# Kernel tuning notes

Measured on AMD Instinct MI355X. Metric: run time of the kernel, lower is better.

## Reference

```python
import jax, jax.numpy as jnp
import numpy as np

DIM = 512
NUM_HEADS = 8
HEAD_DIM = DIM // NUM_HEADS
SCALE = HEAD_DIM ** -0.5
B, T = 8, 1024


def setup_inputs() -> dict:
    key = jax.random.key(0)
    ks = jax.random.split(key, 6)
    x = jax.random.normal(ks[0], (B, T, DIM), dtype=jnp.float32)
    attn_mask = jax.random.randint(ks[1], (B, T, T), 0, 2) == 1  # bool [B,T,T]
    s = 1.0 / np.sqrt(DIM)
    qkv_w = jax.random.uniform(ks[2], (3 * DIM, DIM), jnp.float32, -s, s)
    qkv_b = jax.random.uniform(ks[3], (3 * DIM,), jnp.float32, -s, s)
    proj_w = jax.random.uniform(ks[4], (DIM, DIM), jnp.float32, -s, s)
    proj_b = jax.random.uniform(ks[5], (DIM,), jnp.float32, -s, s)
    return {"x": x, "attn_mask": attn_mask, "qkv_w": qkv_w, "qkv_b": qkv_b,
            "proj_w": proj_w, "proj_b": proj_b}


def reference(x, attn_mask, qkv_w, qkv_b, proj_w, proj_b):
    b, t, c = x.shape
    # QKV projection (torch Linear: x @ W.T + b), split into q,k,v heads
    qkv = x @ qkv_w.T + qkv_b                      # [b,t,3*c]
    qkv = qkv.reshape(b, t, 3, NUM_HEADS, HEAD_DIM)
    qkv = jnp.transpose(qkv, (2, 0, 3, 1, 4))      # [3,b,h,t,d]
    q, k, v = qkv[0], qkv[1], qkv[2]
    scores = jnp.einsum('bhqd,bhkd->bhqk', q, k) * SCALE  # [b,h,t,t]
    min_val = jnp.finfo(scores.dtype).min
    scores = jnp.where(attn_mask[:, None, :, :], min_val, scores)
    attn = jax.nn.softmax(scores, axis=-1)
    out = jnp.einsum('bhqk,bhkd->bhqd', attn, v)   # [b,h,t,d]
    out = jnp.transpose(out, (0, 2, 1, 3)).reshape(b, t, c)
    return out @ proj_w.T + proj_b
```

## Files before the change

kernel.cpp:

```cpp
#include <hip/hip_runtime.h>
#include <math.h>

#define DIM   512
#define NH    8
#define HD    64
#define BATCH 8
#define SEQ   1024
#define QSCALE 0.18033688011112042f

typedef unsigned short u16;
typedef unsigned int   u32;
typedef unsigned long long u64;
typedef __bf16 bf16x8 __attribute__((ext_vector_type(8)));
typedef float  f32x4  __attribute__((ext_vector_type(4)));

__device__ inline u16 f2bf(float f) {
  u32 u = __builtin_bit_cast(u32, f);
  return (u16)((u + 0x7fffu + ((u >> 16) & 1u)) >> 16);
}
__device__ inline float bf2f(u16 h) {
  return __builtin_bit_cast(float, (u32)h << 16);
}
__device__ inline u32 pk2(float a, float b) {
  return (u32)f2bf(a) | ((u32)f2bf(b) << 16);
}

__device__ inline void a16(const u16* g, u16* l) {
  __builtin_amdgcn_global_load_lds(
      (const __attribute__((address_space(1))) u32*)g,
      (__attribute__((address_space(3))) u32*)l, 16, 0, 0);
}


__device__ inline void decomp_body(const float* __restrict__ src, u16* ph,
                                   u16* pl, int t) {
  #pragma unroll
  for (int c = 0; c < 4; ++c) {
    const int cid = c * 256 + t;
    const int row = cid & 15, kc = cid >> 4;
    float f[8];
    *(float4*)&f[0] = *(const float4*)&src[row * DIM + kc * 8];
    *(float4*)&f[4] = *(const float4*)&src[row * DIM + kc * 8 + 4];
    u16 hv[8], lv[8];
    #pragma unroll
    for (int j = 0; j < 8; ++j) {
      hv[j] = f2bf(f[j]);
      lv[j] = f2bf(f[j] - bf2f(hv[j]));
    }
    *(uint4*)&ph[(size_t)cid * 8] = *(const uint4*)hv;
    *(uint4*)&pl[(size_t)cid * 8] = *(const uint4*)lv;
  }
}

__global__ __launch_bounds__(256) void prep(
    const int* __restrict__ mask, u64* __restrict__ bits,
    const float* __restrict__ x, u16* __restrict__ xhi, u16* __restrict__ xlo,
    const float* __restrict__ qkvw, u16* __restrict__ wqh, u16* __restrict__ wql,
    const float* __restrict__ projw, u16* __restrict__ wph, u16* __restrict__ wpl) {
  const int blk = blockIdx.x;
  const int t = threadIdx.x;
  if (blk < 32768) {
    const size_t gid = (size_t)blk * 256 + t;
    const int lane = t & 63;
    const size_t w = gid >> 6;
    const int v = mask[w * 64 + lane];
    const u64 b = __ballot(v != 0);
    if (lane == 0) {
      const int bb = (int)(w >> 14), q = (int)((w >> 4) & 1023),
                kt = (int)(w & 15);
      bits[(((size_t)(bb << 4 | kt)) << 10) | q] = b;
    }
  } else if (blk < 33280) {
    const int rg = blk - 32768;
    decomp_body(x + (size_t)rg * 16 * DIM, xhi + (size_t)rg * 8192,
                xlo + (size_t)rg * 8192, t);
  } else if (blk < 33376) {
    const int rg = blk - 33280;
    decomp_body(qkvw + (size_t)rg * 16 * DIM, wqh + (size_t)rg * 8192,
                wql + (size_t)rg * 8192, t);
  } else {
    const int rg = blk - 33376;
    decomp_body(projw + (size_t)rg * 16 * DIM, wph + (size_t)rg * 8192,
                wpl + (size_t)rg * 8192, t);
  }
}

template <int MB, bool QKV>
__global__ __launch_bounds__(256, 3) void mfma_gemm(
    const u16* __restrict__ Agh, const u16* __restrict__ Agl,
    const u16* __restrict__ Bgh, const u16* __restrict__ Bgl,
    const float* __restrict__ bias, void* __restrict__ out0,
    u16* __restrict__ kfr, u16* __restrict__ vfr) {
  __shared__ u16 sAh[2][MB * 1024];
  __shared__ u16 sAl[2][MB * 1024];

  const int tid = threadIdx.x;
  const int lane = tid & 63;
  const int wv = tid >> 6;
  const int lk = lane & 15, lq = lane >> 4;
  const int m0 = blockIdx.x * (32 * MB), n0 = blockIdx.y * 128;
  const int wm = (wv & 1) * MB;
  const int wn = (wv >> 1) * 4;

  const u16* gAh = Agh + (size_t)(m0 >> 4) * 8192 + lane * 8;
  const u16* gAl = Agl + (size_t)(m0 >> 4) * 8192 + lane * 8;
  const u16* gB0h = Bgh + ((size_t)((n0 >> 4) + wn)) * 8192 + lane * 8;
  const u16* gB0l = Bgl + ((size_t)((n0 >> 4) + wn)) * 8192 + lane * 8;

  auto stageA = [&](int bufi, int ki) {
    #pragma unroll
    for (int it = 0; it < MB / 2; ++it) {
      const int t = it * 4 + wv;
      const size_t go = (size_t)t * 8192 + (size_t)ki * 512;
      const int lo_ = t * 512 + lane * 8;
      a16(gAh + go, &sAh[bufi][lo_]);
      a16(gAl + go, &sAl[bufi][lo_]);
    }
  };

  f32x4 acc[MB][4];
  #pragma unroll
  for (int i = 0; i < MB; ++i)
    #pragma unroll
    for (int j = 0; j < 4; ++j) acc[i][j] = (f32x4){0.f, 0.f, 0.f, 0.f};

  stageA(0, 0);
  __syncthreads();

  #pragma unroll 1
  for (int ki = 0; ki < 16; ++ki) {
    const int cur = ki & 1;
    bf16x8 bh[4], bl[4];
    #pragma unroll
    for (int j = 0; j < 4; ++j) {
      bh[j] = *(const bf16x8*)(gB0h + (size_t)j * 8192 + (size_t)ki * 512);
      bl[j] = *(const bf16x8*)(gB0l + (size_t)j * 8192 + (size_t)ki * 512);
    }
    bf16x8 ah[MB], al[MB];
    #pragma unroll
    for (int i = 0; i < MB; ++i) {
      ah[i] = *(const bf16x8*)&sAh[cur][(wm + i) * 512 + lane * 8];
      al[i] = *(const bf16x8*)&sAl[cur][(wm + i) * 512 + lane * 8];
    }
    if (ki < 15) stageA(cur ^ 1, ki + 1);
    __builtin_amdgcn_sched_barrier(0);

    __builtin_amdgcn_s_setprio(1);
    #pragma unroll
    for (int i = 0; i < MB; ++i)
      #pragma unroll
      for (int j = 0; j < 4; ++j) {
        acc[i][j] = __builtin_amdgcn_mfma_f32_16x16x32_bf16(ah[i], bh[j], acc[i][j], 0, 0, 0);
        acc[i][j] = __builtin_amdgcn_mfma_f32_16x16x32_bf16(ah[i], bl[j], acc[i][j], 0, 0, 0);
        acc[i][j] = __builtin_amdgcn_mfma_f32_16x16x32_bf16(al[i], bh[j], acc[i][j], 0, 0, 0);
      }
    __builtin_amdgcn_s_setprio(0);

    __syncthreads();
  }

  #pragma unroll
  for (int j = 0; j < 4; ++j) {
    const int n = n0 + (wn + j) * 16 + lk;
    const float bv_ = bias[n];
    #pragma unroll
    for (int i = 0; i < MB; ++i) {
      const int mb = m0 + (wm + i) * 16 + lq * 4;
      if (QKV) {
        const int which = n >> 9, h = (n >> 6) & 7, d = n & 63;
        const int b = mb >> 10, tok0 = mb & 1023;
        const size_t hb = (size_t)((b << 3) + h) << 16;
        if (which == 2) {
          const size_t base = hb + ((size_t)(tok0 >> 6) << 12) +
                              ((size_t)((d >> 4) & 3) << 10) +
                              ((size_t)((tok0 >> 5) & 1) << 9) +
                              ((size_t)((d & 15) + (((tok0 >> 3) & 3) << 4)) << 3) +
                              (size_t)(tok0 & 7);
          uint2 o2;
          o2.x = pk2(acc[i][j][0] + bv_, acc[i][j][1] + bv_);
          o2.y = pk2(acc[i][j][2] + bv_, acc[i][j][3] + bv_);
          *(uint2*)&vfr[base] = o2;
        } else if (which == 1) {
          const size_t base = hb + ((size_t)(tok0 >> 4) << 10) +
                              ((size_t)(d >> 5) << 9) + (size_t)(d & 7) +
                              ((size_t)(((d >> 3) & 3) << 4) << 3);
          #pragma unroll
          for (int r = 0; r < 4; ++r)
            kfr[base + (((tok0 & 15) + r) << 3)] = f2bf(acc[i][j][r] + bv_);
        } else {
          u16* dst = (u16*)out0;
          #pragma unroll
          for (int r = 0; r < 4; ++r)
            dst[(((size_t)((b << 3) + h) << 10 | (tok0 + r)) << 6) + d] =
                f2bf((acc[i][j][r] + bv_) * QSCALE);
        }
      } else {
        #pragma unroll
        for (int r = 0; r < 4; ++r)
          ((float*)out0)[(size_t)(mb + r) * DIM + n] = acc[i][j][r] + bv_;
      }
    }
  }
}

__global__ __launch_bounds__(256) void attn_mfma(
    const u16* __restrict__ qg, const u16* __restrict__ kfr,
    const u16* __restrict__ vfr, const u64* __restrict__ bitsT,
    u16* __restrict__ ohi, u16* __restrict__ olo) {
  __shared__ u16 Kls[2][4096];
  __shared__ u16 Vls[2][4096];
  __shared__ u16 Ps[64 * 72];

  const int tid = threadIdx.x;
  const int lane = tid & 63;
  const int wv = tid >> 6;
  const int lk = lane & 15, lq = lane >> 4;
  const int bh = blockIdx.x;
  const int q0 = blockIdx.y * 64;
  const int bb = bh >> 3;
  const int q = q0 + wv * 16 + lk;

  const u16* qrow = qg + ((size_t)(bh << 10 | q) << 6);
  const bf16x8 bq0 = *(const bf16x8*)(qrow + lq * 8);
  const bf16x8 bq1 = *(const bf16x8*)(qrow + 32 + lq * 8);

  const u16* kh = kfr + ((size_t)bh << 16);
  const u16* vh = vfr + ((size_t)bh << 16);
  const u64* bitp = bitsT + ((size_t)bb << 14) + q;
  u16* pw = &Ps[(wv * 16 + lk) * 72];

  auto stage = [&](int bufi, int kt) {
    #pragma unroll
    for (int it = 0; it < 2; ++it) {
      const int c = it * 4 + wv;
      const int off = c * 512 + lane * 8;
      a16(kh + ((size_t)kt << 12) + off, &Kls[bufi][off]);
      a16(vh + ((size_t)kt << 12) + off, &Vls[bufi][off]);
    }
  };

  f32x4 o_[4];
  float l = 0.f;
  #pragma unroll
  for (int t = 0; t < 4; ++t) o_[t] = (f32x4){0.f, 0.f, 0.f, 0.f};

  stage(0, 0);
  __syncthreads();

  #pragma unroll 1
  for (int kt = 0; kt < 16; ++kt) {
    const int cur = kt & 1;
    const u64 wd = bitp[(size_t)kt << 10];

    bf16x8 ak0[4], ak1[4], vb0[4], vb1[4];
    #pragma unroll
    for (int t = 0; t < 4; ++t) {
      ak0[t] = *(const bf16x8*)&Kls[cur][t * 1024 + lane * 8];
      ak1[t] = *(const bf16x8*)&Kls[cur][t * 1024 + 512 + lane * 8];
      vb0[t] = *(const bf16x8*)&Vls[cur][t * 1024 + lane * 8];
      vb1[t] = *(const bf16x8*)&Vls[cur][t * 1024 + 512 + lane * 8];
    }
    if (kt < 15) stage(cur ^ 1, kt + 1);
    __builtin_amdgcn_sched_barrier(0);

    f32x4 st[4];
    const f32x4 z4 = (f32x4){0.f, 0.f, 0.f, 0.f};
    __builtin_amdgcn_s_setprio(1);
    #pragma unroll
    for (int t = 0; t < 4; ++t) {
      f32x4 a = __builtin_amdgcn_mfma_f32_16x16x32_bf16(ak0[t], bq0, z4, 0, 0, 0);
      st[t] = __builtin_amdgcn_mfma_f32_16x16x32_bf16(ak1[t], bq1, a, 0, 0, 0);
    }
    __builtin_amdgcn_s_setprio(0);

    const u32 w0 = (u32)wd, w1 = (u32)(wd >> 32);
    #pragma unroll
    for (int t = 0; t < 4; ++t) {
      const u32 w = (t < 2) ? w0 : w1;
      const int base = (t & 1) * 16 + lq * 4;
      float p[4];
      #pragma unroll
      for (int r = 0; r < 4; ++r) {
        const float sv = ((w >> (base + r)) & 1u) ? -INFINITY : st[t][r];
        p[r] = __builtin_amdgcn_exp2f(sv);
        l += p[r];
      }
      *(uint2*)(pw + t * 16 + lq * 4) = uint2{pk2(p[0], p[1]), pk2(p[2], p[3])};
    }

    const bf16x8 pa0 = *(const bf16x8*)(pw + lq * 8);
    const bf16x8 pa1 = *(const bf16x8*)(pw + 32 + lq * 8);
    __builtin_amdgcn_s_setprio(1);
    #pragma unroll
    for (int t = 0; t < 4; ++t) {
      o_[t] = __builtin_amdgcn_mfma_f32_16x16x32_bf16(pa0, vb0[t], o_[t], 0, 0, 0);
      o_[t] = __builtin_amdgcn_mfma_f32_16x16x32_bf16(pa1, vb1[t], o_[t], 0, 0, 0);
    }
    __builtin_amdgcn_s_setprio(0);

    __syncthreads();
  }

  l += __shfl_xor(l, 16);
  l += __shfl_xor(l, 32);

  const int h = bh & 7;
  #pragma unroll
  for (int r = 0; r < 4; ++r) {
    const float inv = 1.0f / __shfl(l, lq * 4 + r);
    const int tok = q0 + wv * 16 + lq * 4 + r;
    const int m = (bb << 10) | tok;
    const size_t rgo = (size_t)(m >> 4) * 8192 + (size_t)(m & 15) * 8;
    #pragma unroll
    for (int t = 0; t < 4; ++t) {
      const int d = t * 16 + lk;
      const int k = (h << 6) | d;
      const float v = o_[t][r] * inv;
      const u16 hv = f2bf(v);
      const size_t off = rgo + (size_t)(k >> 3) * 128 + (k & 7);
      ohi[off] = hv;
      olo[off] = f2bf(v - bf2f(hv));
    }
  }
}

extern "C" void kernel_launch(void* const* d_in, const int* in_sizes, int n_in,
                              void* d_out, int out_size, void* d_ws,
                              size_t ws_size, hipStream_t stream) {
  const float* x      = (const float*)d_in[0];
  const int*   mask   = (const int*)d_in[1];
  const float* qkv_w  = (const float*)d_in[2];
  const float* qkv_b  = (const float*)d_in[3];
  const float* proj_w = (const float*)d_in[4];
  const float* proj_b = (const float*)d_in[5];
  float* out = (float*)d_out;

  const size_t SZ = (size_t)BATCH * NH * SEQ * HD;
  u64* bits = (u64*)d_ws;
  u16* qb  = (u16*)(bits + 131072);
  u16* kfr = qb + SZ;
  u16* vfr = kfr + SZ;
  u16* xhi = vfr + SZ;
  u16* xlo = xhi + SZ;
  u16* ohi = xlo + SZ;
  u16* olo = ohi + SZ;
  u16* wqh = olo + SZ;
  u16* wql = wqh + 1536 * 512;
  u16* wph = wql + 1536 * 512;
  u16* wpl = wph + 512 * 512;

  prep<<<33408, 256, 0, stream>>>(mask, bits, x, xhi, xlo,
                                  qkv_w, wqh, wql, proj_w, wph, wpl);
  mfma_gemm<4, true><<<dim3(64, 12), 256, 0, stream>>>(
      xhi, xlo, wqh, wql, qkv_b, qb, kfr, vfr);
  attn_mfma<<<dim3(64, SEQ / 64), 256, 0, stream>>>(
      qb, kfr, vfr, bits, ohi, olo);
  mfma_gemm<2, false><<<dim3(128, 4), 256, 0, stream>>>(
      ohi, olo, wph, wpl, proj_b, out, nullptr, nullptr);
}
```

Baseline: 207.4 us.

## Process two query tiles per attention block to reuse K/V fragments

The attention kernel now handles 128 queries per block: each wave computes two 16-query groups that share the same K/V LDS fragments and register loads, and the grid is halved. This amortises the K/V staging, LDS reads and barriers over twice the work, at the cost of more registers and fewer blocks. It also swaps the software bf16 rounding of probabilities for the hardware v_cvt_pk_bf16_f32 instruction.

```diff
diff --git a/kernel.cpp b/kernel.cpp
--- a/kernel.cpp
+++ b/kernel.cpp
@@ -23,6 +23,11 @@
 }
 __device__ inline u32 pk2(float a, float b) {
   return (u32)f2bf(a) | ((u32)f2bf(b) << 16);
+}
+__device__ inline u32 cvtpk(float lo, float hi) {
+  u32 r;
+  asm("v_cvt_pk_bf16_f32 %0, %1, %2" : "=v"(r) : "v"(lo), "v"(hi));
+  return r;
 }
 
 __device__ inline void a16(const u16* g, u16* l) {
@@ -209,25 +214,31 @@
     u16* __restrict__ ohi, u16* __restrict__ olo) {
   __shared__ u16 Kls[2][4096];
   __shared__ u16 Vls[2][4096];
-  __shared__ u16 Ps[64 * 72];
+  __shared__ u16 Ps[128 * 72];
 
   const int tid = threadIdx.x;
   const int lane = tid & 63;
   const int wv = tid >> 6;
   const int lk = lane & 15, lq = lane >> 4;
   const int bh = blockIdx.x;
-  const int q0 = blockIdx.y * 64;
+  const int q0 = blockIdx.y * 128;
   const int bb = bh >> 3;
-  const int q = q0 + wv * 16 + lk;
-
-  const u16* qrow = qg + ((size_t)(bh << 10 | q) << 6);
-  const bf16x8 bq0 = *(const bf16x8*)(qrow + lq * 8);
-  const bf16x8 bq1 = *(const bf16x8*)(qrow + 32 + lq * 8);
+  const int qA = q0 + wv * 16 + lk;
+  const int qB = qA + 64;
+
+  const u16* qrowA = qg + ((size_t)(bh << 10 | qA) << 6);
+  const u16* qrowB = qg + ((size_t)(bh << 10 | qB) << 6);
+  const bf16x8 bqA0 = *(const bf16x8*)(qrowA + lq * 8);
+  const bf16x8 bqA1 = *(const bf16x8*)(qrowA + 32 + lq * 8);
+  const bf16x8 bqB0 = *(const bf16x8*)(qrowB + lq * 8);
+  const bf16x8 bqB1 = *(const bf16x8*)(qrowB + 32 + lq * 8);
 
   const u16* kh = kfr + ((size_t)bh << 16);
   const u16* vh = vfr + ((size_t)bh << 16);
-  const u64* bitp = bitsT + ((size_t)bb << 14) + q;
-  u16* pw = &Ps[(wv * 16 + lk) * 72];
+  const u64* bitpA = bitsT + ((size_t)bb << 14) + qA;
+  const u64* bitpB = bitsT + ((size_t)bb << 14) + qB;
+  u16* pwA = &Ps[(wv * 16 + lk) * 72];
+  u16* pwB = &Ps[(64 + wv * 16 + lk) * 72];
 
   auto stage = [&](int bufi, int kt) {
     #pragma unroll
@@ -239,40 +250,7 @@
     }
   };
 
-  f32x4 o_[4];
-  float l = 0.f;
-  #pragma unroll
-  for (int t = 0; t < 4; ++t) o_[t] = (f32x4){0.f, 0.f, 0.f, 0.f};
-
-  stage(0, 0);
-  __syncthreads();
-
-  #pragma unroll 1
-  for (int kt = 0; kt < 16; ++kt) {
-    const int cur = kt & 1;
-    const u64 wd = bitp[(size_t)kt << 10];
-
-    bf16x8 ak0[4], ak1[4], vb0[4], vb1[4];
-    #pragma unroll
-    for (int t = 0; t < 4; ++t) {
-      ak0[t] = *(const bf16x8*)&Kls[cur][t * 1024 + lane * 8];
-      ak1[t] = *(const bf16x8*)&Kls[cur][t * 1024 + 512 + lane * 8];
-      vb0[t] = *(const bf16x8*)&Vls[cur][t * 1024 + lane * 8];
-      vb1[t] = *(const bf16x8*)&Vls[cur][t * 1024 + 512 + lane * 8];
-    }
-    if (kt < 15) stage(cur ^ 1, kt + 1);
-    __builtin_amdgcn_sched_barrier(0);
-
-    f32x4 st[4];
-    const f32x4 z4 = (f32x4){0.f, 0.f, 0.f, 0.f};
-    __builtin_amdgcn_s_setprio(1);
-    #pragma unroll
-    for (int t = 0; t < 4; ++t) {
-      f32x4 a = __builtin_amdgcn_mfma_f32_16x16x32_bf16(ak0[t], bq0, z4, 0, 0, 0);
-      st[t] = __builtin_amdgcn_mfma_f32_16x16x32_bf16(ak1[t], bq1, a, 0, 0, 0);
-    }
-    __builtin_amdgcn_s_setprio(0);
-
+  auto softmax_store = [&](const f32x4* st, u64 wd, u16* pw, float& l) {
     const u32 w0 = (u32)wd, w1 = (u32)(wd >> 32);
     #pragma unroll
     for (int t = 0; t < 4; ++t) {
@@ -285,43 +263,103 @@
         p[r] = __builtin_amdgcn_exp2f(sv);
         l += p[r];
       }
-      *(uint2*)(pw + t * 16 + lq * 4) = uint2{pk2(p[0], p[1]), pk2(p[2], p[3])};
-    }
-
-    const bf16x8 pa0 = *(const bf16x8*)(pw + lq * 8);
-    const bf16x8 pa1 = *(const bf16x8*)(pw + 32 + lq * 8);
+      *(uint2*)(pw + t * 16 + lq * 4) = uint2{cvtpk(p[0], p[1]), cvtpk(p[2], p[3])};
+    }
+  };
+
+  f32x4 oA[4], oB[4];
+  float lA = 0.f, lB = 0.f;
+  #pragma unroll
+  for (int t = 0; t < 4; ++t) {
+    oA[t] = (f32x4){0.f, 0.f, 0.f, 0.f};
+    oB[t] = (f32x4){0.f, 0.f, 0.f, 0.f};
+  }
+
+  stage(0, 0);
+  __syncthreads();
+
+  #pragma unroll 1
+  for (int kt = 0; kt < 16; ++kt) {
+    const int cur = kt & 1;
+    const u64 wdA = bitpA[(size_t)kt << 10];
+    const u64 wdB = bitpB[(size_t)kt << 10];
+
+    bf16x8 ak0[4], ak1[4], vb0[4], vb1[4];
+    #pragma unroll
+    for (int t = 0; t < 4; ++t) {
+      ak0[t] = *(const bf16x8*)&Kls[cur][t * 1024 + lane * 8];
+      ak1[t] = *(const bf16x8*)&Kls[cur][t * 1024 + 512 + lane * 8];
+      vb0[t] = *(const bf16x8*)&Vls[cur][t * 1024 + lane * 8];
+      vb1[t] = *(const bf16x8*)&Vls[cur][t * 1024 + 512 + lane * 8];
+    }
+    if (kt < 15) stage(cur ^ 1, kt + 1);
+    __builtin_amdgcn_sched_barrier(0);
+
+    const f32x4 z4 = (f32x4){0.f, 0.f, 0.f, 0.f};
+    f32x4 st[4];
+
     __builtin_amdgcn_s_setprio(1);
     #pragma unroll
     for (int t = 0; t < 4; ++t) {
-      o_[t] = __builtin_amdgcn_mfma_f32_16x16x32_bf16(pa0, vb0[t], o_[t], 0, 0, 0);
-      o_[t] = __builtin_amdgcn_mfma_f32_16x16x32_bf16(pa1, vb1[t], o_[t], 0, 0, 0);
+      f32x4 a = __builtin_amdgcn_mfma_f32_16x16x32_bf16(ak0[t], bqA0, z4, 0, 0, 0);
+      st[t] = __builtin_amdgcn_mfma_f32_16x16x32_bf16(ak1[t], bqA1, a, 0, 0, 0);
     }
     __builtin_amdgcn_s_setprio(0);
+    softmax_store(st, wdA, pwA, lA);
+
+    __builtin_amdgcn_s_setprio(1);
+    #pragma unroll
+    for (int t = 0; t < 4; ++t) {
+      f32x4 a = __builtin_amdgcn_mfma_f32_16x16x32_bf16(ak0[t], bqB0, z4, 0, 0, 0);
+      st[t] = __builtin_amdgcn_mfma_f32_16x16x32_bf16(ak1[t], bqB1, a, 0, 0, 0);
+    }
+    __builtin_amdgcn_s_setprio(0);
+    softmax_store(st, wdB, pwB, lB);
+
+    const bf16x8 paA0 = *(const bf16x8*)(pwA + lq * 8);
+    const bf16x8 paA1 = *(const bf16x8*)(pwA + 32 + lq * 8);
+    const bf16x8 paB0 = *(const bf16x8*)(pwB + lq * 8);
+    const bf16x8 paB1 = *(const bf16x8*)(pwB + 32 + lq * 8);
+    __builtin_amdgcn_s_setprio(1);
+    #pragma unroll
+    for (int t = 0; t < 4; ++t) {
+      oA[t] = __builtin_amdgcn_mfma_f32_16x16x32_bf16(paA0, vb0[t], oA[t], 0, 0, 0);
+      oA[t] = __builtin_amdgcn_mfma_f32_16x16x32_bf16(paA1, vb1[t], oA[t], 0, 0, 0);
+      oB[t] = __builtin_amdgcn_mfma_f32_16x16x32_bf16(paB0, vb0[t], oB[t], 0, 0, 0);
+      oB[t] = __builtin_amdgcn_mfma_f32_16x16x32_bf16(paB1, vb1[t], oB[t], 0, 0, 0);
+    }
+    __builtin_amdgcn_s_setprio(0);
 
     __syncthreads();
   }
 
-  l += __shfl_xor(l, 16);
-  l += __shfl_xor(l, 32);
+  lA += __shfl_xor(lA, 16);
+  lA += __shfl_xor(lA, 32);
+  lB += __shfl_xor(lB, 16);
+  lB += __shfl_xor(lB, 32);
 
   const int h = bh & 7;
-  #pragma unroll
-  for (int r = 0; r < 4; ++r) {
-    const float inv = 1.0f / __shfl(l, lq * 4 + r);
-    const int tok = q0 + wv * 16 + lq * 4 + r;
-    const int m = (bb << 10) | tok;
-    const size_t rgo = (size_t)(m >> 4) * 8192 + (size_t)(m & 15) * 8;
-    #pragma unroll
-    for (int t = 0; t < 4; ++t) {
-      const int d = t * 16 + lk;
-      const int k = (h << 6) | d;
-      const float v = o_[t][r] * inv;
-      const u16 hv = f2bf(v);
-      const size_t off = rgo + (size_t)(k >> 3) * 128 + (k & 7);
-      ohi[off] = hv;
-      olo[off] = f2bf(v - bf2f(hv));
-    }
-  }
+  auto epi = [&](const f32x4* o_, float l, int g) {
+    #pragma unroll
+    for (int r = 0; r < 4; ++r) {
+      const float inv = 1.0f / __shfl(l, lq * 4 + r);
+      const int tok = q0 + g * 64 + wv * 16 + lq * 4 + r;
+      const int m = (bb << 10) | tok;
+      const size_t rgo = (size_t)(m >> 4) * 8192 + (size_t)(m & 15) * 8;
+      #pragma unroll
+      for (int t = 0; t < 4; ++t) {
+        const int d = t * 16 + lk;
+        const int k = (h << 6) | d;
+        const float v = o_[t][r] * inv;
+        const u16 hv = f2bf(v);
+        const size_t off = rgo + (size_t)(k >> 3) * 128 + (k & 7);
+        ohi[off] = hv;
+        olo[off] = f2bf(v - bf2f(hv));
+      }
+    }
+  };
+  epi(oA, lA, 0);
+  epi(oB, lB, 1);
 }
 
 extern "C" void kernel_launch(void* const* d_in, const int* in_sizes, int n_in,
@@ -353,7 +391,7 @@
                                   qkv_w, wqh, wql, proj_w, wph, wpl);
   mfma_gemm<4, true><<<dim3(64, 12), 256, 0, stream>>>(
       xhi, xlo, wqh, wql, qkv_b, qb, kfr, vfr);
-  attn_mfma<<<dim3(64, SEQ / 64), 256, 0, stream>>>(
+  attn_mfma<<<dim3(64, SEQ / 128), 256, 0, stream>>>(
       qb, kfr, vfr, bits, ohi, olo);
   mfma_gemm<2, false><<<dim3(128, 4), 256, 0, stream>>>(
       ohi, olo, wph, wpl, proj_b, out, nullptr, nullptr);
```

New measurement: 202.6 us, median of 2. 2.3% less time.
